# Kernel optimization log

Measured on AMD Instinct MI355X. Metric: run time of the kernel, lower is better.

Reference implementation:

```python
import jax, jax.numpy as jnp
import numpy as np

N_NODES = 50000
N_RELS = 8
IN_DIM = 128
OUT_DIM = 128
N_EDGES = 800000


def setup_inputs() -> dict:
    key = jax.random.key(0)
    k1, k2, k3, k4 = jax.random.split(key, 4)
    src = jax.random.randint(k1, (N_EDGES,), 0, N_NODES, dtype=jnp.int64 if jax.config.jax_enable_x64 else jnp.int32)
    rel = jax.random.randint(k2, (N_EDGES,), 0, N_RELS, dtype=src.dtype)
    tgt = jax.random.randint(k3, (N_EDGES,), 0, N_NODES, dtype=src.dtype)
    triples = jnp.stack([src, rel, tgt], axis=1)  # (E, 3) like torch layout (s, r, t)
    features = jax.random.normal(k4, (N_NODES, IN_DIM), dtype=jnp.float32)
    weights = jax.random.normal(jax.random.fold_in(key, 1), (N_RELS, IN_DIM, OUT_DIM), dtype=jnp.float32) * (1.0 / np.sqrt(IN_DIM))
    bias = jnp.zeros((OUT_DIM,), dtype=jnp.float32)
    return {"triples": triples, "features": features, "weights": weights, "bias": bias}


def reference(triples, features, weights, bias):
    # RGCN-NC forward, horizontal stacking (featured mode):
    #   out[t] = sum_{(s,r,t) in E} (1/c_{t,r}) * features[s] @ W[r] + bias
    # where c_{t,r} = #edges sharing the same (relation, target) pair,
    # matching sum_sparse(..., row_normalisation=False) on the (n x r*n) adjacency.
    src, rel, tgt = triples[:, 0], triples[:, 1], triples[:, 2]
    n = features.shape[0]
    r = weights.shape[0]
    e = triples.shape[0]

    # per-(rel, tgt) edge counts -> 1/c normalization per edge
    key = rel * n + tgt  # column index of horizontally stacked adjacency
    counts = jax.ops.segment_sum(jnp.ones((e,), dtype=features.dtype), key, num_segments=r * n)
    vals = 1.0 / counts[key]  # (E,)

    # dense per-relation transform: H[r] = X @ W[r]   (r, n, out)
    h = jnp.einsum('ni,rio->rno', features, weights)

    # gather per-edge messages, scale, scatter-add into targets
    msgs = h[rel, src] * vals[:, None]  # (E, out)
    out = jax.ops.segment_sum(msgs, tgt, num_segments=n)  # (n, out)
    return out + bias
```

## Files before the change

kernel.cpp:

```cpp
#include <hip/hip_runtime.h>
#include <hip/hip_bf16.h>

#define N_NODES 50000
#define N_RELS 8
#define IN_DIM 128
#define OUT_DIM 128
#define N_EDGES 800000
#define NR (N_NODES * N_RELS)
#define KDIM (N_RELS * IN_DIM)
#define SCAN_ELEMS 2048
#define SCAN_NBLK ((NR + SCAN_ELEMS - 1) / SCAN_ELEMS)
#define M_PAD 50048
#define CNT_BLKS ((N_EDGES / 4 + 255) / 256)
#define CW_BLKS ((N_RELS * IN_DIM * OUT_DIM + 255) / 256)
#define FB_BLKS ((N_NODES * IN_DIM / 8 + 255) / 256)

typedef __attribute__((ext_vector_type(8))) short bf16x8;
typedef __attribute__((ext_vector_type(4))) float floatx4;

__device__ inline unsigned short f2bf(float f) {
    unsigned u = __builtin_bit_cast(unsigned, f);
    u += 0x7fff + ((u >> 16) & 1);
    return (unsigned short)(u >> 16);
}
__device__ inline float bflo(unsigned u) {
    return __builtin_bit_cast(float, u << 16);
}
__device__ inline float bfhi(unsigned u) {
    return __builtin_bit_cast(float, u & 0xffff0000u);
}

__global__ void prep_kernel(const int* __restrict__ tri, const float* __restrict__ W,
                            const float* __restrict__ features,
                            int* __restrict__ cnt, unsigned short* __restrict__ Wtf,
                            unsigned short* __restrict__ featB) {
    const int b = blockIdx.x;
    if (b < CNT_BLKS) {
        int t = b * 256 + threadIdx.x;
        if (t >= N_EDGES / 4) return;
        const int4* tri4 = (const int4*)tri;
        int4 a = tri4[3 * t], v = tri4[3 * t + 1], c = tri4[3 * t + 2];
        atomicAdd(&cnt[a.z * N_RELS + a.y], 1);
        atomicAdd(&cnt[v.y * N_RELS + v.x], 1);
        atomicAdd(&cnt[c.x * N_RELS + v.w], 1);
        atomicAdd(&cnt[c.w * N_RELS + c.z], 1);
    } else if (b < CNT_BLKS + CW_BLKS) {
        int idx = (b - CNT_BLKS) * 256 + threadIdx.x;
        if (idx >= N_RELS * IN_DIM * OUT_DIM) return;
        int e  = idx & 7;
        int l  = (idx >> 3) & 63;
        int ks = (idx >> 9) & 31;
        int nt = idx >> 14;
        int o = nt * 16 + (l & 15);
        int k = ks * 32 + (l >> 4) * 8 + e;
        Wtf[idx] = f2bf(W[(k >> 7) * (IN_DIM * OUT_DIM) + (k & 127) * OUT_DIM + o]);
    } else {
        int t = (b - CNT_BLKS - CW_BLKS) * 256 + threadIdx.x;
        if (t >= N_NODES * IN_DIM / 8) return;
        const float4* f4 = (const float4*)features;
        float4 x = f4[2 * t], y = f4[2 * t + 1];
        uint4 o;
        o.x = (unsigned)f2bf(x.x) | ((unsigned)f2bf(x.y) << 16);
        o.y = (unsigned)f2bf(x.z) | ((unsigned)f2bf(x.w) << 16);
        o.z = (unsigned)f2bf(y.x) | ((unsigned)f2bf(y.y) << 16);
        o.w = (unsigned)f2bf(y.z) | ((unsigned)f2bf(y.w) << 16);
        ((uint4*)featB)[t] = o;
    }
}

__global__ void scan_part(const int* __restrict__ cnt, int* __restrict__ bsum) {
    __shared__ int s[256];
    int b = blockIdx.x, t = threadIdx.x;
    int base = b * SCAN_ELEMS + t * 8;
    int sum = 0;
#pragma unroll
    for (int k = 0; k < 8; ++k) {
        int i = base + k;
        sum += (i < NR) ? cnt[i] : 0;
    }
    s[t] = sum; __syncthreads();
    for (int off = 128; off > 0; off >>= 1) {
        if (t < off) s[t] += s[t + off];
        __syncthreads();
    }
    if (t == 0) bsum[b] = s[0];
}

__global__ void scan_mid(const int* __restrict__ bsum, int* __restrict__ boff) {
    __shared__ int s[256];
    int t = threadIdx.x;
    int v = (t < SCAN_NBLK) ? bsum[t] : 0;
    s[t] = v; __syncthreads();
    for (int off = 1; off < 256; off <<= 1) {
        int x = (t >= off) ? s[t - off] : 0;
        __syncthreads();
        s[t] += x;
        __syncthreads();
    }
    if (t < SCAN_NBLK) boff[t] = s[t] - v;
}

__global__ void scan_apply(const int* __restrict__ cnt, const int* __restrict__ boff,
                           int* __restrict__ segOff, int* __restrict__ cursor) {
    __shared__ int s[256];
    int b = blockIdx.x, t = threadIdx.x;
    int base = b * SCAN_ELEMS + t * 8;
    int v[8]; int sum = 0;
#pragma unroll
    for (int k = 0; k < 8; ++k) {
        int i = base + k;
        v[k] = (i < NR) ? cnt[i] : 0;
        sum += v[k];
    }
    s[t] = sum; __syncthreads();
    for (int off = 1; off < 256; off <<= 1) {
        int x = (t >= off) ? s[t - off] : 0;
        __syncthreads();
        s[t] += x;
        __syncthreads();
    }
    int run = boff[b] + s[t] - sum;
#pragma unroll
    for (int k = 0; k < 8; ++k) {
        int i = base + k;
        if (i < NR) { segOff[i] = run; cursor[i] = run; run += v[k]; }
    }
    if (b == 0 && t == 0) segOff[NR] = N_EDGES;
}

__global__ void scatter_kernel(const int* __restrict__ tri, int* __restrict__ cursor,
                               int* __restrict__ sortedSrc) {
    int e = blockIdx.x * 256 + threadIdx.x;
    if (e >= N_EDGES) return;
    int src = tri[3 * e];
    int rel = tri[3 * e + 1];
    int tgt = tri[3 * e + 2];
    int p = atomicAdd(&cursor[tgt * N_RELS + rel], 1);
    sortedSrc[p] = src;
}

__global__ __launch_bounds__(256) void agg_kernel(
    const int* __restrict__ sortedSrc, const int* __restrict__ segOff,
    const unsigned short* __restrict__ featB, unsigned short* __restrict__ aggG)
{
    const int wave = threadIdx.x >> 6, lane = threadIdx.x & 63;
    const int node = blockIdx.x * 4 + wave;
    const int h = lane >> 5, l = lane & 31;

    int bnd = 0;
    if (lane < 9) bnd = segOff[node * N_RELS + lane];
    int s[9];
#pragma unroll
    for (int i = 0; i < 9; ++i) s[i] = __shfl(bnd, i);

    const int e0 = s[0], eN = s[8];
    int srcw = 0;
    if (e0 + lane < eN) srcw = sortedSrc[e0 + lane];

    const unsigned short* fb = featB + 4 * l;
    unsigned short* dst = aggG + (size_t)node * KDIM + 4 * l;

#pragma unroll
    for (int p = 0; p < 4; ++p) {
        const int r = 2 * p + h;
        const int s0v = s[r], s1v = s[r + 1];
        const int len = s1v - s0v;
        const int olen = __shfl_xor(len, 32);
        const int jmax = (len > olen) ? len : olen;
        float a0 = 0.f, a1 = 0.f, a2 = 0.f, a3 = 0.f;
        for (int j = 0; j < jmax; ++j) {
            const int e = s0v + j;
            const int i0 = e - e0;
            const int swin = __shfl(srcw, i0 & 63);
            if (j < len) {
                const int src = (i0 < 64) ? swin : sortedSrc[e];
                uint2 u = *(const uint2*)&fb[src * IN_DIM];
                a0 += bflo(u.x); a1 += bfhi(u.x);
                a2 += bflo(u.y); a3 += bfhi(u.y);
            }
        }
        const float inv = (len > 0) ? 1.0f / (float)len : 0.0f;
        uint2 pk;
        pk.x = (unsigned)f2bf(a0 * inv) | ((unsigned)f2bf(a1 * inv) << 16);
        pk.y = (unsigned)f2bf(a2 * inv) | ((unsigned)f2bf(a3 * inv) << 16);
        *(uint2*)&dst[r * IN_DIM] = pk;
    }
}

__global__ __launch_bounds__(256) void gemm_kernel(
    const unsigned short* __restrict__ aggG,
    const unsigned short* __restrict__ Wtf,
    const float* __restrict__ bias,
    float* __restrict__ out)
{
    __shared__ unsigned short Abuf[64 * 128];
    const int tid = threadIdx.x;
    const int wave = tid >> 6, lane = tid & 63;
    const int qk = lane >> 4, ln16 = lane & 15;
    const int m0 = blockIdx.x * 64;
    const int wm = wave & 1, wn = wave >> 1;

    floatx4 acc[2][4];
#pragma unroll
    for (int st = 0; st < 2; ++st)
#pragma unroll
        for (int nt = 0; nt < 4; ++nt) acc[st][nt] = (floatx4){0.f, 0.f, 0.f, 0.f};

    const int l4 = lane >> 4, l15 = lane & 15;

    for (int c = 0; c < 8; ++c) {
        __syncthreads();
#pragma unroll
        for (int i = 0; i < 4; ++i) {
            const int row = wave * 16 + i * 4 + l4;
            const int unit = l15 ^ (row & 15);
            const unsigned short* g =
                aggG + (size_t)(m0 + row) * KDIM + c * 128 + unit * 8;
            __builtin_amdgcn_global_load_lds(
                (const __attribute__((address_space(1))) unsigned int*)g,
                (__attribute__((address_space(3))) unsigned int*)&Abuf[(wave * 16 + i * 4) * 128],
                16, 0, 0);
        }
        __syncthreads();

#pragma unroll
        for (int ksl = 0; ksl < 4; ++ksl) {
            const int ks = c * 4 + ksl;
            bf16x8 a[2];
#pragma unroll
            for (int st = 0; st < 2; ++st) {
                const int r = wm * 32 + st * 16 + ln16;
                const int u = (ksl * 4 + qk) ^ (r & 15);
                a[st] = *(const bf16x8*)&Abuf[r * 128 + u * 8];
            }
#pragma unroll
            for (int nt = 0; nt < 4; ++nt) {
                const int ntg = wn * 4 + nt;
                bf16x8 b = *(const bf16x8*)&Wtf[(size_t)((ntg * 32 + ks) * 64 + lane) * 8];
                acc[0][nt] = __builtin_amdgcn_mfma_f32_16x16x32_bf16(a[0], b, acc[0][nt], 0, 0, 0);
                acc[1][nt] = __builtin_amdgcn_mfma_f32_16x16x32_bf16(a[1], b, acc[1][nt], 0, 0, 0);
            }
        }
    }

#pragma unroll
    for (int nt = 0; nt < 4; ++nt) {
        const int o = (wn * 4 + nt) * 16 + ln16;
        const float bv = bias[o];
#pragma unroll
        for (int st = 0; st < 2; ++st)
#pragma unroll
            for (int j = 0; j < 4; ++j) {
                const int t = m0 + wm * 32 + st * 16 + qk * 4 + j;
                if (t < N_NODES) out[(size_t)t * OUT_DIM + o] = acc[st][nt][j] + bv;
            }
    }
}

extern "C" void kernel_launch(void* const* d_in, const int* in_sizes, int n_in,
                              void* d_out, int out_size, void* d_ws, size_t ws_size,
                              hipStream_t stream)
{
    const int*   tri      = (const int*)d_in[0];
    const float* features = (const float*)d_in[1];
    const float* W        = (const float*)d_in[2];
    const float* bias     = (const float*)d_in[3];
    float* out = (float*)d_out;

    char* ws = (char*)d_ws;
    unsigned short* Wtf = (unsigned short*)ws; ws += (size_t)OUT_DIM * KDIM * 2;
    int* cnt       = (int*)ws; ws += (size_t)NR * 4;
    int* segOff    = (int*)ws; ws += (size_t)(NR + 4) * 4;
    int* cursor    = (int*)ws; ws += (size_t)NR * 4;
    int* bsum      = (int*)ws; ws += (size_t)SCAN_NBLK * 4;
    int* boff      = (int*)ws; ws += (size_t)SCAN_NBLK * 4;
    int* sortedSrc = (int*)ws; ws += (size_t)N_EDGES * 4;
    unsigned short* featB = (unsigned short*)ws; ws += (size_t)N_NODES * IN_DIM * 2;
    unsigned short* aggG  = (unsigned short*)ws; ws += (size_t)M_PAD * KDIM * 2;
    (void)ws_size; (void)in_sizes; (void)n_in; (void)out_size;

    hipMemsetAsync(cnt, 0, NR * sizeof(int), stream);
    prep_kernel<<<CNT_BLKS + CW_BLKS + FB_BLKS, 256, 0, stream>>>(tri, W, features, cnt, Wtf, featB);
    scan_part<<<SCAN_NBLK, 256, 0, stream>>>(cnt, bsum);
    scan_mid<<<1, 256, 0, stream>>>(bsum, boff);
    scan_apply<<<SCAN_NBLK, 256, 0, stream>>>(cnt, boff, segOff, cursor);
    scatter_kernel<<<(N_EDGES + 255) / 256, 256, 0, stream>>>(tri, cursor, sortedSrc);
    agg_kernel<<<N_NODES / 4, 256, 0, stream>>>(sortedSrc, segOff, featB, aggG);
    gemm_kernel<<<M_PAD / 64, 256, 0, stream>>>(aggG, Wtf, bias, out);
}
```

Before: 274.0 us.

## Fuse three-pass scan into decoupled look-back scan; widen agg loads to 16B

Replaces the three scan kernels (part, mid, apply) with a single-pass decoupled look-back scan that publishes block aggregates and prefix flags through global atomics. This removes two launches and a reread of the count array. Separately, the aggregation kernel now gives each lane 8 bf16 features via uint4 loads, with four relations handled per wave pass instead of two. The look-back relies on blocks being scheduled in order to avoid spinning, and the wider agg layout takes the max segment length over four relations, which can increase divergence.

New measurement: 303.4 us. 1.11x slower.

```diff
diff --git a/kernel.cpp b/kernel.cpp
--- a/kernel.cpp
+++ b/kernel.cpp
@@ -68,43 +68,14 @@
     }
 }
 
-__global__ void scan_part(const int* __restrict__ cnt, int* __restrict__ bsum) {
+__global__ __launch_bounds__(256) void scan_kernel(
+    const int* __restrict__ cnt, unsigned* __restrict__ flags,
+    int* __restrict__ segOff, int* __restrict__ cursor)
+{
     __shared__ int s[256];
-    int b = blockIdx.x, t = threadIdx.x;
-    int base = b * SCAN_ELEMS + t * 8;
-    int sum = 0;
-#pragma unroll
-    for (int k = 0; k < 8; ++k) {
-        int i = base + k;
-        sum += (i < NR) ? cnt[i] : 0;
-    }
-    s[t] = sum; __syncthreads();
-    for (int off = 128; off > 0; off >>= 1) {
-        if (t < off) s[t] += s[t + off];
-        __syncthreads();
-    }
-    if (t == 0) bsum[b] = s[0];
-}
-
-__global__ void scan_mid(const int* __restrict__ bsum, int* __restrict__ boff) {
-    __shared__ int s[256];
-    int t = threadIdx.x;
-    int v = (t < SCAN_NBLK) ? bsum[t] : 0;
-    s[t] = v; __syncthreads();
-    for (int off = 1; off < 256; off <<= 1) {
-        int x = (t >= off) ? s[t - off] : 0;
-        __syncthreads();
-        s[t] += x;
-        __syncthreads();
-    }
-    if (t < SCAN_NBLK) boff[t] = s[t] - v;
-}
-
-__global__ void scan_apply(const int* __restrict__ cnt, const int* __restrict__ boff,
-                           int* __restrict__ segOff, int* __restrict__ cursor) {
-    __shared__ int s[256];
-    int b = blockIdx.x, t = threadIdx.x;
-    int base = b * SCAN_ELEMS + t * 8;
+    __shared__ int sbase;
+    const int b = blockIdx.x, t = threadIdx.x;
+    const int base = b * SCAN_ELEMS + t * 8;
     int v[8]; int sum = 0;
 #pragma unroll
     for (int k = 0; k < 8; ++k) {
@@ -119,7 +90,32 @@
         s[t] += x;
         __syncthreads();
     }
-    int run = boff[b] + s[t] - sum;
+    if (t == 0) {
+        const int blockAgg = s[255];
+        if (b == 0) {
+            __hip_atomic_store(&flags[0], ((unsigned)blockAgg << 2) | 2u,
+                               __ATOMIC_RELEASE, __HIP_MEMORY_SCOPE_AGENT);
+            sbase = 0;
+        } else {
+            __hip_atomic_store(&flags[b], ((unsigned)blockAgg << 2) | 1u,
+                               __ATOMIC_RELEASE, __HIP_MEMORY_SCOPE_AGENT);
+            int acc = 0, p = b - 1;
+            while (true) {
+                unsigned f = __hip_atomic_load(&flags[p], __ATOMIC_ACQUIRE,
+                                               __HIP_MEMORY_SCOPE_AGENT);
+                unsigned st = f & 3u;
+                if (st == 0u) continue;
+                acc += (int)(f >> 2);
+                if (st == 2u) break;
+                --p;
+            }
+            __hip_atomic_store(&flags[b], (((unsigned)(acc + blockAgg)) << 2) | 2u,
+                               __ATOMIC_RELEASE, __HIP_MEMORY_SCOPE_AGENT);
+            sbase = acc;
+        }
+    }
+    __syncthreads();
+    int run = sbase + s[t] - sum;
 #pragma unroll
     for (int k = 0; k < 8; ++k) {
         int i = base + k;
@@ -145,7 +141,7 @@
 {
     const int wave = threadIdx.x >> 6, lane = threadIdx.x & 63;
     const int node = blockIdx.x * 4 + wave;
-    const int h = lane >> 5, l = lane & 31;
+    const int q = lane >> 4, l16 = lane & 15;
 
     int bnd = 0;
     if (lane < 9) bnd = segOff[node * N_RELS + lane];
@@ -157,33 +153,40 @@
     int srcw = 0;
     if (e0 + lane < eN) srcw = sortedSrc[e0 + lane];
 
-    const unsigned short* fb = featB + 4 * l;
-    unsigned short* dst = aggG + (size_t)node * KDIM + 4 * l;
-
-#pragma unroll
-    for (int p = 0; p < 4; ++p) {
-        const int r = 2 * p + h;
+    const unsigned short* fb = featB + 8 * l16;
+    unsigned short* dst = aggG + (size_t)node * KDIM + 8 * l16;
+
+#pragma unroll
+    for (int p = 0; p < 2; ++p) {
+        const int r = 4 * p + q;
         const int s0v = s[r], s1v = s[r + 1];
         const int len = s1v - s0v;
-        const int olen = __shfl_xor(len, 32);
-        const int jmax = (len > olen) ? len : olen;
+        int m0x = __shfl_xor(len, 16);
+        int jm = (len > m0x) ? len : m0x;
+        int m1x = __shfl_xor(jm, 32);
+        const int jmax = (jm > m1x) ? jm : m1x;
         float a0 = 0.f, a1 = 0.f, a2 = 0.f, a3 = 0.f;
+        float a4 = 0.f, a5 = 0.f, a6 = 0.f, a7 = 0.f;
         for (int j = 0; j < jmax; ++j) {
             const int e = s0v + j;
             const int i0 = e - e0;
             const int swin = __shfl(srcw, i0 & 63);
             if (j < len) {
                 const int src = (i0 < 64) ? swin : sortedSrc[e];
-                uint2 u = *(const uint2*)&fb[src * IN_DIM];
+                uint4 u = *(const uint4*)&fb[src * IN_DIM];
                 a0 += bflo(u.x); a1 += bfhi(u.x);
                 a2 += bflo(u.y); a3 += bfhi(u.y);
+                a4 += bflo(u.z); a5 += bfhi(u.z);
+                a6 += bflo(u.w); a7 += bfhi(u.w);
             }
         }
         const float inv = (len > 0) ? 1.0f / (float)len : 0.0f;
-        uint2 pk;
+        uint4 pk;
         pk.x = (unsigned)f2bf(a0 * inv) | ((unsigned)f2bf(a1 * inv) << 16);
         pk.y = (unsigned)f2bf(a2 * inv) | ((unsigned)f2bf(a3 * inv) << 16);
-        *(uint2*)&dst[r * IN_DIM] = pk;
+        pk.z = (unsigned)f2bf(a4 * inv) | ((unsigned)f2bf(a5 * inv) << 16);
+        pk.w = (unsigned)f2bf(a6 * inv) | ((unsigned)f2bf(a7 * inv) << 16);
+        *(uint4*)&dst[r * IN_DIM] = pk;
     }
 }
 
@@ -269,21 +272,18 @@
 
     char* ws = (char*)d_ws;
     unsigned short* Wtf = (unsigned short*)ws; ws += (size_t)OUT_DIM * KDIM * 2;
-    int* cnt       = (int*)ws; ws += (size_t)NR * 4;
-    int* segOff    = (int*)ws; ws += (size_t)(NR + 4) * 4;
-    int* cursor    = (int*)ws; ws += (size_t)NR * 4;
-    int* bsum      = (int*)ws; ws += (size_t)SCAN_NBLK * 4;
-    int* boff      = (int*)ws; ws += (size_t)SCAN_NBLK * 4;
-    int* sortedSrc = (int*)ws; ws += (size_t)N_EDGES * 4;
+    int* cnt        = (int*)ws;      ws += (size_t)NR * 4;
+    unsigned* flags = (unsigned*)ws; ws += 256 * 4;
+    int* segOff     = (int*)ws;      ws += (size_t)(NR + 4) * 4;
+    int* cursor     = (int*)ws;      ws += (size_t)NR * 4;
+    int* sortedSrc  = (int*)ws;      ws += (size_t)N_EDGES * 4;
     unsigned short* featB = (unsigned short*)ws; ws += (size_t)N_NODES * IN_DIM * 2;
     unsigned short* aggG  = (unsigned short*)ws; ws += (size_t)M_PAD * KDIM * 2;
     (void)ws_size; (void)in_sizes; (void)n_in; (void)out_size;
 
-    hipMemsetAsync(cnt, 0, NR * sizeof(int), stream);
+    hipMemsetAsync(cnt, 0, (NR + 256) * sizeof(int), stream);
     prep_kernel<<<CNT_BLKS + CW_BLKS + FB_BLKS, 256, 0, stream>>>(tri, W, features, cnt, Wtf, featB);
-    scan_part<<<SCAN_NBLK, 256, 0, stream>>>(cnt, bsum);
-    scan_mid<<<1, 256, 0, stream>>>(bsum, boff);
-    scan_apply<<<SCAN_NBLK, 256, 0, stream>>>(cnt, boff, segOff, cursor);
+    scan_kernel<<<SCAN_NBLK, 256, 0, stream>>>(cnt, flags, segOff, cursor);
     scatter_kernel<<<(N_EDGES + 255) / 256, 256, 0, stream>>>(tri, cursor, sortedSrc);
     agg_kernel<<<N_NODES / 4, 256, 0, stream>>>(sortedSrc, segOff, featB, aggG);
     gemm_kernel<<<M_PAD / 64, 256, 0, stream>>>(aggG, Wtf, bias, out);
```
